# Kernel tuning notes

Hardware: AMD Instinct MI355X
Metric: run time of the kernel (lower is better)

The kernel has to match this reference:

```python
import jax, jax.numpy as jnp
import numpy as np

N, E, G = 10000, 100000, 64
NB, EMB, S, COUT, LMAX = 16, 16, 8, 16, 2
RMAX = 4.0
WNUM = (LMAX + 1) * COUT * S * S  # 3072 per-edge TP weights


def setup_inputs() -> dict:
    key = jax.random.key(0)
    ks = jax.random.split(key, 16)
    def lin(k, i, o):
        return (jax.random.normal(k, (i, o), jnp.float32) / np.sqrt(i)).astype(jnp.float32)
    return {
        "pos": jax.random.normal(ks[0], (N, 3), jnp.float32),
        "A": jax.random.randint(ks[1], (N,), 0, 10),
        "batch": jnp.sort(jax.random.randint(ks[2], (N,), 0, G)),
        "edge_src": jax.random.randint(ks[3], (E,), 0, N),
        "edge_dst": jax.random.randint(ks[4], (E,), 0, N),
        "edge_shifts": jnp.zeros((E, 3), jnp.float32),
        "cell": jax.random.normal(ks[5], (G, 3, 3), jnp.float32),
        "emb_table": jax.random.normal(ks[6], (10, EMB), jnp.float32),
        "mlp_w1": lin(ks[7], EMB, 64), "mlp_b1": jnp.zeros((64,), jnp.float32),
        "mlp_w2": lin(ks[8], 64, S), "mlp_b2": jnp.zeros((S,), jnp.float32),
        "fc_w1": lin(ks[9], NB, 64), "fc_b1": jnp.zeros((64,), jnp.float32),
        "fc_w2": lin(ks[10], 64, 64), "fc_b2": jnp.zeros((64,), jnp.float32),
        "fc_w3": lin(ks[11], 64, WNUM), "fc_b3": jnp.zeros((WNUM,), jnp.float32),
    }


def _forward(pos, edge_shifts, cell, emb_table, mlp_w1, mlp_b1, mlp_w2, mlp_b2,
             fc_w1, fc_b1, fc_w2, fc_b2, fc_w3, fc_b3, A, batch, edge_src, edge_dst):
    # periodic-image edge vectors: shifts @ cell[graph of src node]
    shift = jnp.einsum('ei,eij->ej', edge_shifts, cell[batch[edge_src]])
    vec = pos[edge_dst] - pos[edge_src] + shift                     # (E,3)
    r = jnp.linalg.norm(vec, axis=1)                                # (E,)
    n = vec / jnp.maximum(r, 1e-9)[:, None]                         # unit edge direction
    # per-node scalar features: atom_mlp(atom_embedding(A))
    Ai = jax.nn.silu(emb_table[A] @ mlp_w1 + mlp_b1) @ mlp_w2 + mlp_b2  # (N,S)
    # radial basis: gaussian soft-one-hot on [0, RMAX] with cutoff, * sqrt(NB)
    vals = jnp.linspace(0.0, RMAX, NB + 2)[1:-1]
    step = RMAX / (NB + 1)
    emb = jnp.exp(-(((r[:, None] - vals) / step) ** 2)) / 1.12 * np.sqrt(NB)  # (E,NB)
    # radial MLP -> per-edge tensor-product weights
    h = jax.nn.silu(emb @ fc_w1 + fc_b1)
    h = jax.nn.silu(h @ fc_w2 + fc_b2)
    W = (h @ fc_w3 + fc_b3).reshape(E, LMAX + 1, COUT, S, S)        # (E,L,Cout,C1,C2)
    # f_in rank-L block is Ai[src] x n^{(x)L}; x2 is scalar Ai[dst].
    # The Cartesian TP factorizes: channel mixing once, then attach n^{(x)L}.
    fs, fd = Ai[edge_src], Ai[edge_dst]                             # (E,S)
    m = jnp.einsum('eloab,ea,eb->elo', W, fs, fd)                   # (E,L,Cout)
    out0 = m[:, 0]                                                  # (E,Cout)       rank 0
    out1 = m[:, 1, :, None] * n[:, None, :]                         # (E,Cout,3)     rank 1
    n2 = n[:, :, None] * n[:, None, :]                              # (E,3,3)
    out2 = m[:, 2, :, None, None] * n2[:, None]                     # (E,Cout,3,3)   rank 2
    ef = jnp.concatenate([out0, out1.reshape(E, -1), out2.reshape(E, -1)], axis=-1)  # (E, 13*Cout)
    # scatter-sum to destination nodes, normalize by neighbor count (clamped to 1)
    cnt = jnp.maximum(jax.ops.segment_sum(jnp.ones((E,), ef.dtype), edge_dst, num_segments=N), 1.0)
    return jax.ops.segment_sum(ef, edge_dst, num_segments=N) / cnt[:, None]  # (N, 208)


def reference(pos, A, batch, edge_src, edge_dst, edge_shifts, cell, emb_table,
              mlp_w1, mlp_b1, mlp_w2, mlp_b2, fc_w1, fc_b1, fc_w2, fc_b2, fc_w3, fc_b3):
    return _forward(pos, edge_shifts, cell, emb_table, mlp_w1, mlp_b1, mlp_w2, mlp_b2,
                    fc_w1, fc_b1, fc_w2, fc_b2, fc_w3, fc_b3, A, batch, edge_src, edge_dst)
```

## Files before the change

kernel.cpp:

```cpp
#include <hip/hip_runtime.h>
#include <math.h>
#include <stdint.h>


typedef float  f32x4  __attribute__((ext_vector_type(4)));
typedef short  s16x8  __attribute__((ext_vector_type(8)));
typedef __bf16 bf16x8 __attribute__((ext_vector_type(8)));

__device__ __forceinline__ float silu_f(float x) {
    return x / (1.0f + __expf(-x));
}

__device__ __forceinline__ void split8(f32x4 a, f32x4 b, s16x8& hi, s16x8& lo) {
    bf16x8 h8, l8;
    #pragma unroll
    for (int i = 0; i < 4; ++i) {
        float z = a[i]; __bf16 zh = (__bf16)z; h8[i] = zh; l8[i] = (__bf16)(z - (float)zh);
        float y = b[i]; __bf16 yh = (__bf16)y; h8[4 + i] = yh; l8[4 + i] = (__bf16)(y - (float)yh);
    }
    hi = __builtin_bit_cast(s16x8, h8);
    lo = __builtin_bit_cast(s16x8, l8);
}

__global__ __launch_bounds__(256) void k_setup(const float* __restrict__ w3,
                                               const float* __restrict__ b3,
                                               ushort* __restrict__ wz,
                                               const int* __restrict__ A,
                                               const float* __restrict__ embt,
                                               const float* __restrict__ w1,
                                               const float* __restrict__ b1,
                                               const float* __restrict__ w2,
                                               const float* __restrict__ b2,
                                               float* __restrict__ Ai,
                                               const int* __restrict__ edst,
                                               int* __restrict__ deg,
                                               int N, int E, int aiB) {
    const int b = blockIdx.x;
    const int tid = threadIdx.x;
    if (b < 780) {
        int t = b * 256 + tid;
        int j    = t & 7;
        int l    = (t >> 3) & 63;
        int rest = t >> 9;
        int tt   = rest % 3;
        int s    = rest / 3;
        int lo   = tt * 16 + (l & 15);
        int kl   = (l >> 4) * 8 + j;
        float v;
        if (s < 128) {
            int ab = s >> 1;
            int c  = (s & 1) * 32 + kl;
            v = w3[c * 3072 + lo * 64 + ab];
        } else {
            int ab = (s - 128) * 32 + kl;
            v = b3[lo * 64 + ab];
        }
        __bf16 hi  = (__bf16)v;
        __bf16 lor = (__bf16)(v - (float)hi);
        size_t base = (size_t)(s * 3 + tt) * 2 * 512 + l * 8 + j;
        wz[base]       = __builtin_bit_cast(ushort, hi);
        wz[base + 512] = __builtin_bit_cast(ushort, lor);
    } else if (b < 780 + aiB) {
        int i = (b - 780) * 256 + tid;
        if (i >= N) return;
        float e[16];
        const float* er = embt + A[i] * 16;
        #pragma unroll
        for (int k = 0; k < 16; ++k) e[k] = er[k];
        float h1[64];
        #pragma unroll
        for (int j = 0; j < 64; ++j) {
            float a = b1[j];
            #pragma unroll
            for (int k = 0; k < 16; ++k) a = fmaf(e[k], w1[k * 64 + j], a);
            h1[j] = silu_f(a);
        }
        #pragma unroll
        for (int o = 0; o < 8; ++o) {
            float a = b2[o];
            #pragma unroll
            for (int j = 0; j < 64; ++j) a = fmaf(h1[j], w2[j * 8 + o], a);
            Ai[i * 8 + o] = a;
        }
    } else {
        int e = (b - 780 - aiB) * 256 + tid;
        if (e < E) atomicAdd(&deg[edst[e]], 1);
    }
}

__global__ __launch_bounds__(1024) void k_scan(const int* __restrict__ deg,
                                               int* __restrict__ offs,
                                               int* __restrict__ cursor, int N) {
    __shared__ int part[1024];
    const int t = threadIdx.x;
    const int chunk = (N + 1023) / 1024;
    const int beg = t * chunk;
    const int end = min(beg + chunk, N);
    int s = 0;
    for (int i = beg; i < end; ++i) s += deg[i];
    part[t] = s;
    __syncthreads();
    for (int off = 1; off < 1024; off <<= 1) {
        int v = (t >= off) ? part[t - off] : 0;
        __syncthreads();
        part[t] += v;
        __syncthreads();
    }
    int run = (t == 0) ? 0 : part[t - 1];
    for (int i = beg; i < end; ++i) {
        offs[i] = run;
        cursor[i] = run;
        run += deg[i];
    }
    if (t == 1023) offs[N] = part[1023];
}

__global__ __launch_bounds__(256, 2) void k_edge(
    const float* __restrict__ pos, const int* __restrict__ batch,
    const int* __restrict__ esrc, const int* __restrict__ edst,
    const float* __restrict__ eshift, const float* __restrict__ cell,
    const float* __restrict__ fw1, const float* __restrict__ fb1,
    const float* __restrict__ fw2, const float* __restrict__ fb2,
    const ushort* __restrict__ wz,
    const float* __restrict__ Ai, float* __restrict__ ef,
    int* __restrict__ cursor, int* __restrict__ eidx, int E) {

    __shared__ __align__(16) float s_un[8704];
    __shared__ __align__(16) float s_o[8704];

    const int tid  = threadIdx.x;
    const int lane = tid & 63;
    const int w    = __builtin_amdgcn_readfirstlane(tid >> 6);
    const int e0   = blockIdx.x * 128;
    const int j0   = w * 16;

    const f32x4* wzv = reinterpret_cast<const f32x4*>(wz);

    s16x8 Ba[12], Bb[12];
#define LOADB(ARR, U) { \
    const f32x4* gs = wzv + (size_t)(U) * 768 + lane; \
    _Pragma("unroll") \
    for (int f = 0; f < 12; ++f) ARR[f] = __builtin_bit_cast(s16x8, gs[f * 64]); }

    LOADB(Ba, 0);

    #pragma unroll
    for (int rr = 0; rr < 2; ++rr) {
        const int e = e0 + rr * 64 + lane;
        const bool valid = (e < E);
        const int ec = valid ? e : (E - 1);
        const int src = esrc[ec];
        const int dst = edst[ec];

        const int g0 = batch[src];
        const float s0 = eshift[ec * 3 + 0], s1 = eshift[ec * 3 + 1], s2 = eshift[ec * 3 + 2];
        const float* cl = cell + g0 * 9;
        float vx = pos[dst * 3 + 0] - pos[src * 3 + 0] + s0 * cl[0] + s1 * cl[3] + s2 * cl[6];
        float vy = pos[dst * 3 + 1] - pos[src * 3 + 1] + s0 * cl[1] + s1 * cl[4] + s2 * cl[7];
        float vz = pos[dst * 3 + 2] - pos[src * 3 + 2] + s0 * cl[2] + s1 * cl[5] + s2 * cl[8];
        float r = sqrtf(vx * vx + vy * vy + vz * vz);
        float rinv = 1.0f / fmaxf(r, 1e-9f);
        float nx = vx * rinv, ny = vy * rinv, nz = vz * rinv;

        float embv[16];
        const float step = 4.0f / 17.0f;
        const float sc = 4.0f / 1.12f;
        #pragma unroll
        for (int k = 0; k < 16; ++k) {
            float d = (r - (float)(k + 1) * step) / step;
            embv[k] = __expf(-d * d) * sc;
        }

        const int hb = (rr * 64 + lane) * 65;
        #pragma unroll
        for (int jj = 0; jj < 16; ++jj) {
            const int j = j0 + jj;
            float a = fb1[j];
            #pragma unroll
            for (int k = 0; k < 16; ++k) a = fmaf(embv[k], fw1[k * 64 + j], a);
            s_un[hb + j] = silu_f(a);
        }

        {
            const float* As = Ai + (size_t)src * 8;
            const float* Ad = Ai + (size_t)dst * 8;
            float fsa0 = As[2 * w], fsa1 = As[2 * w + 1];
            f32x4 d0 = *reinterpret_cast<const f32x4*>(Ad);
            f32x4 d1 = *reinterpret_cast<const f32x4*>(Ad + 4);
            float fdv[8] = {d0[0], d0[1], d0[2], d0[3], d1[0], d1[1], d1[2], d1[3]};
            const int ob = (rr * 64 + lane) * 68 + j0;
            #pragma unroll
            for (int i = 0; i < 8; ++i)  s_o[ob + i]     = fsa0 * fdv[i];
            #pragma unroll
            for (int i = 0; i < 8; ++i)  s_o[ob + 8 + i] = fsa1 * fdv[i];
        }

        if (w == 0 && valid) {
            float* np = ef + (size_t)e * 52;
            np[48] = nx; np[49] = ny; np[50] = nz;
            int pp = atomicAdd(&cursor[dst], 1);
            eidx[pp] = e;
        }
    }
    __syncthreads();

    float hcr[2][16];
    #pragma unroll
    for (int rr = 0; rr < 2; ++rr) {
        const int hb = (rr * 64 + lane) * 65;
        #pragma unroll
        for (int i = 0; i < 16; ++i) hcr[rr][i] = fb2[j0 + i];
        #pragma unroll 4
        for (int j = 0; j < 64; ++j) {
            const float v = s_un[hb + j];
            const float* w2r = fw2 + j * 64 + j0;
            #pragma unroll
            for (int i = 0; i < 16; ++i) hcr[rr][i] = fmaf(v, w2r[i], hcr[rr][i]);
        }
        #pragma unroll
        for (int i = 0; i < 16; ++i) hcr[rr][i] = silu_f(hcr[rr][i]);
    }
    __syncthreads();

    #pragma unroll
    for (int rr = 0; rr < 2; ++rr) {
        const int hb = (rr * 64 + lane) * 68 + j0;
        #pragma unroll
        for (int i = 0; i < 16; ++i) s_un[hb + i] = hcr[rr][i];
    }
    __syncthreads();

    LOADB(Bb, 64);

    const int g = lane >> 4;
    const int mrow = w * 32 + (lane & 15);
    s16x8 AhF[2][2], AlF[2][2], OhF[2][2], OlF[2][2];
    #pragma unroll
    for (int mt = 0; mt < 2; ++mt) {
        const float* hr = s_un + (mrow + mt * 16) * 68;
        const float* orw = s_o + (mrow + mt * 16) * 68;
        f32x4 a0 = *reinterpret_cast<const f32x4*>(hr + g * 8);
        f32x4 a1 = *reinterpret_cast<const f32x4*>(hr + g * 8 + 4);
        split8(a0, a1, AhF[mt][0], AlF[mt][0]);
        f32x4 a2 = *reinterpret_cast<const f32x4*>(hr + 32 + g * 8);
        f32x4 a3 = *reinterpret_cast<const f32x4*>(hr + 32 + g * 8 + 4);
        split8(a2, a3, AhF[mt][1], AlF[mt][1]);
        f32x4 o0 = *reinterpret_cast<const f32x4*>(orw + g * 8);
        f32x4 o1 = *reinterpret_cast<const f32x4*>(orw + g * 8 + 4);
        split8(o0, o1, OhF[mt][0], OlF[mt][0]);
        f32x4 o2 = *reinterpret_cast<const f32x4*>(orw + 32 + g * 8);
        f32x4 o3 = *reinterpret_cast<const f32x4*>(orw + 32 + g * 8 + 4);
        split8(o2, o3, OhF[mt][1], OlF[mt][1]);
    }

    const int rb = w * 32 + (lane >> 4) * 4;

    f32x4 acc[2][3];
    #pragma unroll
    for (int mt = 0; mt < 2; ++mt)
        #pragma unroll
        for (int t = 0; t < 3; ++t) acc[mt][t] = (f32x4){0.f, 0.f, 0.f, 0.f};

    __builtin_amdgcn_s_setprio(1);
    #pragma unroll
    for (int t = 0; t < 3; ++t) {
        #pragma unroll
        for (int sl = 0; sl < 2; ++sl) {
            s16x8 Bh = Bb[(sl * 3 + t) * 2];
            s16x8 Bl = Bb[(sl * 3 + t) * 2 + 1];
            acc[0][t] = __builtin_amdgcn_mfma_f32_16x16x32_bf16(OhF[0][sl], Bh, acc[0][t], 0, 0, 0);
            acc[0][t] = __builtin_amdgcn_mfma_f32_16x16x32_bf16(OhF[0][sl], Bl, acc[0][t], 0, 0, 0);
            acc[0][t] = __builtin_amdgcn_mfma_f32_16x16x32_bf16(OlF[0][sl], Bh, acc[0][t], 0, 0, 0);
            acc[1][t] = __builtin_amdgcn_mfma_f32_16x16x32_bf16(OhF[1][sl], Bh, acc[1][t], 0, 0, 0);
            acc[1][t] = __builtin_amdgcn_mfma_f32_16x16x32_bf16(OhF[1][sl], Bl, acc[1][t], 0, 0, 0);
            acc[1][t] = __builtin_amdgcn_mfma_f32_16x16x32_bf16(OlF[1][sl], Bh, acc[1][t], 0, 0, 0);
        }
    }
    __builtin_amdgcn_s_setprio(0);

#define MSTEP(BC, U) { \
    float ov[8]; \
    _Pragma("unroll") \
    for (int i = 0; i < 4; ++i) { \
        ov[i]     = s_o[(rb + i) * 68 + (U)]; \
        ov[4 + i] = s_o[(rb + 16 + i) * 68 + (U)]; \
    } \
    f32x4 D0 = {0.f, 0.f, 0.f, 0.f}, D1 = {0.f, 0.f, 0.f, 0.f}; \
    f32x4 D2 = {0.f, 0.f, 0.f, 0.f}, D3 = {0.f, 0.f, 0.f, 0.f}; \
    f32x4 D4 = {0.f, 0.f, 0.f, 0.f}, D5 = {0.f, 0.f, 0.f, 0.f}; \
    __builtin_amdgcn_s_setprio(1); \
    _Pragma("unroll") \
    for (int sl = 0; sl < 2; ++sl) { \
        s16x8 Bh0 = BC[(sl * 3 + 0) * 2], Bl0 = BC[(sl * 3 + 0) * 2 + 1]; \
        s16x8 Bh1 = BC[(sl * 3 + 1) * 2], Bl1 = BC[(sl * 3 + 1) * 2 + 1]; \
        s16x8 Bh2 = BC[(sl * 3 + 2) * 2], Bl2 = BC[(sl * 3 + 2) * 2 + 1]; \
        D0 = __builtin_amdgcn_mfma_f32_16x16x32_bf16(AhF[0][sl], Bh0, D0, 0, 0, 0); \
        D1 = __builtin_amdgcn_mfma_f32_16x16x32_bf16(AhF[1][sl], Bh0, D1, 0, 0, 0); \
        D2 = __builtin_amdgcn_mfma_f32_16x16x32_bf16(AhF[0][sl], Bh1, D2, 0, 0, 0); \
        D3 = __builtin_amdgcn_mfma_f32_16x16x32_bf16(AhF[1][sl], Bh1, D3, 0, 0, 0); \
        D4 = __builtin_amdgcn_mfma_f32_16x16x32_bf16(AhF[0][sl], Bh2, D4, 0, 0, 0); \
        D5 = __builtin_amdgcn_mfma_f32_16x16x32_bf16(AhF[1][sl], Bh2, D5, 0, 0, 0); \
        D0 = __builtin_amdgcn_mfma_f32_16x16x32_bf16(AlF[0][sl], Bh0, D0, 0, 0, 0); \
        D1 = __builtin_amdgcn_mfma_f32_16x16x32_bf16(AlF[1][sl], Bh0, D1, 0, 0, 0); \
        D2 = __builtin_amdgcn_mfma_f32_16x16x32_bf16(AlF[0][sl], Bh1, D2, 0, 0, 0); \
        D3 = __builtin_amdgcn_mfma_f32_16x16x32_bf16(AlF[1][sl], Bh1, D3, 0, 0, 0); \
        D4 = __builtin_amdgcn_mfma_f32_16x16x32_bf16(AlF[0][sl], Bh2, D4, 0, 0, 0); \
        D5 = __builtin_amdgcn_mfma_f32_16x16x32_bf16(AlF[1][sl], Bh2, D5, 0, 0, 0); \
        D0 = __builtin_amdgcn_mfma_f32_16x16x32_bf16(AhF[0][sl], Bl0, D0, 0, 0, 0); \
        D1 = __builtin_amdgcn_mfma_f32_16x16x32_bf16(AhF[1][sl], Bl0, D1, 0, 0, 0); \
        D2 = __builtin_amdgcn_mfma_f32_16x16x32_bf16(AhF[0][sl], Bl1, D2, 0, 0, 0); \
        D3 = __builtin_amdgcn_mfma_f32_16x16x32_bf16(AhF[1][sl], Bl1, D3, 0, 0, 0); \
        D4 = __builtin_amdgcn_mfma_f32_16x16x32_bf16(AhF[0][sl], Bl2, D4, 0, 0, 0); \
        D5 = __builtin_amdgcn_mfma_f32_16x16x32_bf16(AhF[1][sl], Bl2, D5, 0, 0, 0); \
    } \
    __builtin_amdgcn_s_setprio(0); \
    _Pragma("unroll") \
    for (int i = 0; i < 4; ++i) { \
        acc[0][0][i] = fmaf(ov[i],     D0[i], acc[0][0][i]); \
        acc[1][0][i] = fmaf(ov[4 + i], D1[i], acc[1][0][i]); \
        acc[0][1][i] = fmaf(ov[i],     D2[i], acc[0][1][i]); \
        acc[1][1][i] = fmaf(ov[4 + i], D3[i], acc[1][1][i]); \
        acc[0][2][i] = fmaf(ov[i],     D4[i], acc[0][2][i]); \
        acc[1][2][i] = fmaf(ov[4 + i], D5[i], acc[1][2][i]); \
    } }

    for (int u = 0; u < 64; u += 2) {
        LOADB(Bb, u + 1);
        MSTEP(Ba, u);
        if (u + 2 < 64) LOADB(Ba, u + 2);
        MSTEP(Bb, u + 1);
    }
#undef MSTEP
#undef LOADB

    #pragma unroll
    for (int mt = 0; mt < 2; ++mt) {
        #pragma unroll
        for (int t = 0; t < 3; ++t) {
            #pragma unroll
            for (int i = 0; i < 4; ++i) {
                const int ee = e0 + rb + mt * 16 + i;
                if (ee < E) ef[(size_t)ee * 52 + t * 16 + (lane & 15)] = acc[mt][t][i];
            }
        }
    }
}

__global__ __launch_bounds__(256) void k_gather(const float* __restrict__ ef,
                                                const int* __restrict__ offs,
                                                const int* __restrict__ eidx,
                                                float* __restrict__ out, int N) {
    const int lane = threadIdx.x & 63;
    const int node = blockIdx.x * 4 + (threadIdx.x >> 6);
    if (node >= N) return;

    const int beg = offs[node];
    const int end = offs[node + 1];

    int mi[4], ii[4], jj[4], mode[4];
    #pragma unroll
    for (int t = 0; t < 4; ++t) {
        int c = lane + 64 * t;
        if (c < 16)       { mi[t] = c;                 ii[t] = 0;     jj[t] = 0;     mode[t] = 0; }
        else if (c < 64)  { int u = c - 16; mi[t] = 16 + u / 3; ii[t] = u % 3; jj[t] = 0; mode[t] = 1; }
        else if (c < 208) { int u = c - 64; mi[t] = 32 + u / 9; int rr = u % 9; ii[t] = rr / 3; jj[t] = rr % 3; mode[t] = 2; }
        else              { mi[t] = 0; ii[t] = 0; jj[t] = 0; mode[t] = 3; }
    }

    float acc[4] = {0.f, 0.f, 0.f, 0.f};
    #pragma unroll 4
    for (int k = beg; k < end; ++k) {
        const int e = eidx[k];
        const float* b = ef + (size_t)e * 52;
        float v = (lane < 51) ? b[lane] : 0.0f;
        float n0 = __shfl(v, 48);
        float n1 = __shfl(v, 49);
        float n2 = __shfl(v, 50);
        #pragma unroll
        for (int t = 0; t < 4; ++t) {
            float mval = __shfl(v, mi[t]);
            float ni = (ii[t] == 0) ? n0 : ((ii[t] == 1) ? n1 : n2);
            float nj = (jj[t] == 0) ? n0 : ((jj[t] == 1) ? n1 : n2);
            float f  = (mode[t] == 0) ? 1.0f
                     : (mode[t] == 1) ? ni
                     : (mode[t] == 2) ? ni * nj
                     : 0.0f;
            acc[t] = fmaf(mval, f, acc[t]);
        }
    }

    const float inv = 1.0f / fmaxf((float)(end - beg), 1.0f);
    float* op = out + (size_t)node * 208;
    op[lane]        = acc[0] * inv;
    op[lane + 64]   = acc[1] * inv;
    op[lane + 128]  = acc[2] * inv;
    if (lane < 16) op[lane + 192] = acc[3] * inv;
}

extern "C" void kernel_launch(void* const* d_in, const int* in_sizes, int n_in,
                              void* d_out, int out_size, void* d_ws, size_t ws_size,
                              hipStream_t stream) {
    const float* pos    = (const float*)d_in[0];
    const int*   A      = (const int*)d_in[1];
    const int*   batch  = (const int*)d_in[2];
    const int*   esrc   = (const int*)d_in[3];
    const int*   edst   = (const int*)d_in[4];
    const float* eshift = (const float*)d_in[5];
    const float* cell   = (const float*)d_in[6];
    const float* embt   = (const float*)d_in[7];
    const float* mw1    = (const float*)d_in[8];
    const float* mb1    = (const float*)d_in[9];
    const float* mw2    = (const float*)d_in[10];
    const float* mb2    = (const float*)d_in[11];
    const float* fw1    = (const float*)d_in[12];
    const float* fb1    = (const float*)d_in[13];
    const float* fw2    = (const float*)d_in[14];
    const float* fb2    = (const float*)d_in[15];
    const float* w3     = (const float*)d_in[16];
    const float* b3     = (const float*)d_in[17];
    float* out = (float*)d_out;

    const int N = in_sizes[1];
    const int E = in_sizes[3];

    char* p = (char*)d_ws;
    auto take = [&](size_t bytes) {
        char* q = p;
        p += (bytes + 255) & ~(size_t)255;
        return q;
    };
    ushort* wz    = (ushort*)take((size_t)130 * 3 * 2 * 512 * sizeof(ushort));
    float* Ai     = (float*)take((size_t)N * 8 * sizeof(float));
    int*   deg    = (int*)  take((size_t)N * sizeof(int));
    int*   offs   = (int*)  take((size_t)(N + 1) * sizeof(int));
    int*   cursor = (int*)  take((size_t)N * sizeof(int));
    int*   eidx   = (int*)  take((size_t)E * sizeof(int));
    float* ef     = (float*)take((size_t)E * 52 * sizeof(float));

    hipMemsetAsync(deg, 0, (size_t)N * sizeof(int), stream);

    const int aiB = (N + 255) / 256;
    const int histB = (E + 255) / 256;
    k_setup<<<780 + aiB + histB, 256, 0, stream>>>(w3, b3, wz, A, embt, mw1, mb1,
                                                   mw2, mb2, Ai, edst, deg, N, E, aiB);
    k_scan<<<1, 1024, 0, stream>>>(deg, offs, cursor, N);
    k_edge<<<(E + 127) / 128, 256, 0, stream>>>(pos, batch, esrc, edst, eshift, cell,
                                                fw1, fb1, fw2, fb2, wz, Ai,
                                                ef, cursor, eidx, E);
    k_gather<<<(N + 3) / 4, 256, 0, stream>>>(ef, offs, eidx, out, N);
}
```

Measured before the change: 245.9 us.

## Write edge features in destination-sorted slots and coalesce weight repack reads

The edge kernel now claims its CSR slot with the atomic before the tensor-product work, keeps it in shared memory, and writes edge features straight into destination-sorted order. The gather kernel then reads contiguous rows with no index indirection, and the eidx array is dropped. The setup weight repack is also changed to read w3/b3 linearly, so its global loads coalesce while its writes scatter instead. The cost is scattered stores from the edge kernel in place of the gather's scattered loads.

```diff
diff --git a/kernel.cpp b/kernel.cpp
--- a/kernel.cpp
+++ b/kernel.cpp
@@ -37,27 +37,36 @@
                                                int N, int E, int aiB) {
     const int b = blockIdx.x;
     const int tid = threadIdx.x;
-    if (b < 780) {
-        int t = b * 256 + tid;
-        int j    = t & 7;
-        int l    = (t >> 3) & 63;
-        int rest = t >> 9;
-        int tt   = rest % 3;
-        int s    = rest / 3;
-        int lo   = tt * 16 + (l & 15);
-        int kl   = (l >> 4) * 8 + j;
-        float v;
-        if (s < 128) {
-            int ab = s >> 1;
-            int c  = (s & 1) * 32 + kl;
-            v = w3[c * 3072 + lo * 64 + ab];
-        } else {
-            int ab = (s - 128) * 32 + kl;
-            v = b3[lo * 64 + ab];
-        }
+    if (b < 768) {
+        const int idx = b * 256 + tid;
+        const int c   = idx / 3072;
+        const int rem = idx - c * 3072;
+        const int lo  = rem >> 6;
+        const int ab  = rem & 63;
+        const float v = w3[idx];
+        const int s  = (ab << 1) | (c >> 5);
+        const int kl = c & 31;
+        const int j  = kl & 7;
+        const int l  = ((kl >> 3) << 4) | (lo & 15);
+        const int tt = lo >> 4;
         __bf16 hi  = (__bf16)v;
         __bf16 lor = (__bf16)(v - (float)hi);
-        size_t base = (size_t)(s * 3 + tt) * 2 * 512 + l * 8 + j;
+        const size_t base = (size_t)(s * 3 + tt) * 2 * 512 + l * 8 + j;
+        wz[base]       = __builtin_bit_cast(ushort, hi);
+        wz[base + 512] = __builtin_bit_cast(ushort, lor);
+    } else if (b < 780) {
+        const int i2 = (b - 768) * 256 + tid;
+        const int lo = i2 >> 6;
+        const int ab = i2 & 63;
+        const float v = b3[i2];
+        const int s  = 128 + (ab >> 5);
+        const int kl = ab & 31;
+        const int j  = kl & 7;
+        const int l  = ((kl >> 3) << 4) | (lo & 15);
+        const int tt = lo >> 4;
+        __bf16 hi  = (__bf16)v;
+        __bf16 lor = (__bf16)(v - (float)hi);
+        const size_t base = (size_t)(s * 3 + tt) * 2 * 512 + l * 8 + j;
         wz[base]       = __builtin_bit_cast(ushort, hi);
         wz[base + 512] = __builtin_bit_cast(ushort, lor);
     } else if (b < 780 + aiB) {
@@ -123,10 +132,11 @@
     const float* __restrict__ fw2, const float* __restrict__ fb2,
     const ushort* __restrict__ wz,
     const float* __restrict__ Ai, float* __restrict__ ef,
-    int* __restrict__ cursor, int* __restrict__ eidx, int E) {
+    int* __restrict__ cursor, int E) {
 
     __shared__ __align__(16) float s_un[8704];
     __shared__ __align__(16) float s_o[8704];
+    __shared__ int s_pos[128];
 
     const int tid  = threadIdx.x;
     const int lane = tid & 63;
@@ -196,10 +206,10 @@
         }
 
         if (w == 0 && valid) {
-            float* np = ef + (size_t)e * 52;
+            int pp = atomicAdd(&cursor[dst], 1);
+            s_pos[rr * 64 + lane] = pp;
+            float* np = ef + (size_t)pp * 52;
             np[48] = nx; np[49] = ny; np[50] = nz;
-            int pp = atomicAdd(&cursor[dst], 1);
-            eidx[pp] = e;
         }
     }
     __syncthreads();
@@ -335,12 +345,15 @@
 
     #pragma unroll
     for (int mt = 0; mt < 2; ++mt) {
+        const int row = rb + mt * 16;
         #pragma unroll
         for (int t = 0; t < 3; ++t) {
             #pragma unroll
             for (int i = 0; i < 4; ++i) {
-                const int ee = e0 + rb + mt * 16 + i;
-                if (ee < E) ef[(size_t)ee * 52 + t * 16 + (lane & 15)] = acc[mt][t][i];
+                if (e0 + row + i < E) {
+                    const int pp = s_pos[row + i];
+                    ef[(size_t)pp * 52 + t * 16 + (lane & 15)] = acc[mt][t][i];
+                }
             }
         }
     }
@@ -348,7 +361,6 @@
 
 __global__ __launch_bounds__(256) void k_gather(const float* __restrict__ ef,
                                                 const int* __restrict__ offs,
-                                                const int* __restrict__ eidx,
                                                 float* __restrict__ out, int N) {
     const int lane = threadIdx.x & 63;
     const int node = blockIdx.x * 4 + (threadIdx.x >> 6);
@@ -370,8 +382,7 @@
     float acc[4] = {0.f, 0.f, 0.f, 0.f};
     #pragma unroll 4
     for (int k = beg; k < end; ++k) {
-        const int e = eidx[k];
-        const float* b = ef + (size_t)e * 52;
+        const float* b = ef + (size_t)k * 52;
         float v = (lane < 51) ? b[lane] : 0.0f;
         float n0 = __shfl(v, 48);
         float n1 = __shfl(v, 49);
@@ -434,7 +445,6 @@
     int*   deg    = (int*)  take((size_t)N * sizeof(int));
     int*   offs   = (int*)  take((size_t)(N + 1) * sizeof(int));
     int*   cursor = (int*)  take((size_t)N * sizeof(int));
-    int*   eidx   = (int*)  take((size_t)E * sizeof(int));
     float* ef     = (float*)take((size_t)E * 52 * sizeof(float));
 
     hipMemsetAsync(deg, 0, (size_t)N * sizeof(int), stream);
@@ -446,6 +456,6 @@
     k_scan<<<1, 1024, 0, stream>>>(deg, offs, cursor, N);
     k_edge<<<(E + 127) / 128, 256, 0, stream>>>(pos, batch, esrc, edst, eshift, cell,
                                                 fw1, fb1, fw2, fb2, wz, Ai,
-                                                ef, cursor, eidx, E);
-    k_gather<<<(N + 3) / 4, 256, 0, stream>>>(ef, offs, eidx, out, N);
-}
+                                                ef, cursor, E);
+    k_gather<<<(N + 3) / 4, 256, 0, stream>>>(ef, offs, out, N);
+}
```

New measurement: 237.5 us. 1.04x faster.
